# Kernel tuning notes

Measured on AMD Instinct MI355X. Metric: run time of the kernel, lower is better.

Reference implementation:

```python
import jax, jax.numpy as jnp
import numpy as np

B, D, K = 8192, 512, 4096
MAX_WORD_LENGTH = 16
RESIDUAL_THRESHOLD = 0.01
DECAY_FACTOR = 0.95
EPS_TARGET = 1e-8


def setup_inputs() -> dict:
    key = jax.random.key(0)
    k1, k2 = jax.random.split(key)
    targets = jax.random.normal(k1, (B, D), dtype=jnp.float32)
    codebook = jax.random.normal(k2, (K, D), dtype=jnp.float32)
    return {"targets": targets, "codebook": codebook}


def reference(targets, codebook):
    """Batched greedy residual pursuit (allow_negative_signs=True).

    Returns:
      seq      [B, L] int32 signed indices (>=0: add idx; <0: subtract (-idx-1)); 0 where inactive
      mask     [B, L] bool, True where a step actually emitted a symbol
      residual [B, D] final residual after pursuit
    """
    target_norm = jnp.linalg.norm(targets, axis=-1)  # [B]

    def step(residual, step_idx):
        rnorm = jnp.linalg.norm(residual, axis=-1)  # [B]
        active = (rnorm >= RESIDUAL_THRESHOLD) & (target_norm >= EPS_TARGET)
        # cosine similarity of each codebook vector with residual direction
        res_dir = residual / jnp.maximum(rnorm, 1e-12)[:, None]
        cos = jnp.einsum('bd,kd->bk', res_dir, codebook)  # [B, K]
        best = jnp.argmax(jnp.abs(cos), axis=-1)  # [B]
        best_cos = jnp.take_along_axis(cos, best[:, None], axis=-1)[:, 0]
        signed = jnp.where(best_cos >= 0, best, -(best + 1)).astype(jnp.int32)
        sign = jnp.where(best_cos >= 0, 1.0, -1.0).astype(residual.dtype)
        decay = jnp.power(jnp.asarray(DECAY_FACTOR, residual.dtype),
                          (step_idx + 1).astype(residual.dtype))
        contrib = sign[:, None] * decay * codebook[best]  # [B, D]
        new_res = jnp.where(active[:, None], residual - contrib, residual)
        out_idx = jnp.where(active, signed, 0)
        return new_res, (out_idx, active)

    residual, (seq, mask) = jax.lax.scan(step, targets, jnp.arange(MAX_WORD_LENGTH))
    return seq.T, mask.T, residual
```

## Files before the change

### kernel.cpp

```cpp
#include <hip/hip_runtime.h>
#include <hip/hip_bf16.h>

#define B_SZ 8192
#define D_SZ 512
#define K_SZ 4096
#define L_SZ 16
#define M_ALL (B_SZ + K_SZ)

typedef __attribute__((ext_vector_type(8))) short short8v;
typedef __attribute__((ext_vector_type(4))) float f32x4;
typedef _Float16 half8v __attribute__((ext_vector_type(8)));
typedef _Float16 h2 __attribute__((ext_vector_type(2)));
struct H2x4 { h2 a, b, c, d; };

typedef const __attribute__((address_space(1))) void gvoid;
typedef __attribute__((address_space(3))) void lvoid;

static __device__ __forceinline__ h2 habs2(h2 a) {
    unsigned u = __builtin_bit_cast(unsigned, a) & 0x7FFF7FFFu;
    return __builtin_bit_cast(h2, u);
}
static __device__ __forceinline__ h2 hmax2(h2 a, h2 b) {
#if __has_builtin(__builtin_elementwise_max)
    return __builtin_elementwise_max(a, b);
#else
    h2 r; r[0] = a[0] > b[0] ? a[0] : b[0]; r[1] = a[1] > b[1] ? a[1] : b[1]; return r;
#endif
}

__global__ void cast_bf16_kernel(const float* __restrict__ targets,
                                 const float* __restrict__ codebook,
                                 __hip_bfloat16* __restrict__ abf) {
    int idx = blockIdx.x * blockDim.x + threadIdx.x;
    const int total4 = (M_ALL * D_SZ) / 4;
    if (idx >= total4) return;
    int base = idx * 4;
    const float* src = (base < B_SZ * D_SZ) ? (targets + base)
                                            : (codebook + (base - B_SZ * D_SZ));
    float4 v = *(const float4*)src;
    abf[base + 0] = __float2bfloat16(v.x);
    abf[base + 1] = __float2bfloat16(v.y);
    abf[base + 2] = __float2bfloat16(v.z);
    abf[base + 3] = __float2bfloat16(v.w);
}

__global__ void cn2_kernel(const float* __restrict__ codebook,
                           double* __restrict__ cn2) {
    int row  = blockIdx.x * 4 + (threadIdx.x >> 6);
    int lane = threadIdx.x & 63;
    const float* r = codebook + (size_t)row * D_SZ;
    double s = 0.0;
#pragma unroll
    for (int j = 0; j < 8; j++) { double v = (double)r[lane + 64 * j]; s += v * v; }
#pragma unroll
    for (int o = 32; o > 0; o >>= 1) s += __shfl_down(s, o, 64);
    if (lane == 0) cn2[row] = s;
}

#define BM 128
#define BN 128
#define BK 32

__global__ __launch_bounds__(256)
void gemm_bt_kernel(const __hip_bfloat16* __restrict__ A,
                    const __hip_bfloat16* __restrict__ Bm,
                    _Float16* __restrict__ C) {
    __shared__ short As[BM * BK];
    __shared__ short Bs[BN * BK];
    const int tid  = threadIdx.x;
    const int bm   = blockIdx.y * BM;
    const int bn   = blockIdx.x * BN;
    const int wave = tid >> 6, lane = tid & 63;
    const int wm = (wave & 1) * 64, wn = (wave >> 1) * 64;
    const int row16 = lane & 15, quad = lane >> 4;
    const int koff = quad * 8;

    f32x4 acc[4][4] = {};

    const short* Ag = (const short*)A;
    const short* Bg = (const short*)Bm;
    const int srow = lane >> 2;
    const int scol = (lane & 3) * 8;

    for (int k0 = 0; k0 < D_SZ; k0 += BK) {
        __syncthreads();
#pragma unroll
        for (int c = 0; c < 2; c++) {
            int row = (wave * 2 + c) * 16 + srow;
            __builtin_amdgcn_global_load_lds(
                (gvoid*)(Ag + (size_t)(bm + row) * D_SZ + k0 + scol),
                (lvoid*)(As + row * BK + scol), 16, 0, 0);
            __builtin_amdgcn_global_load_lds(
                (gvoid*)(Bg + (size_t)(bn + row) * D_SZ + k0 + scol),
                (lvoid*)(Bs + row * BK + scol), 16, 0, 0);
        }
        __syncthreads();

        short8v af[4], bf[4];
#pragma unroll
        for (int i = 0; i < 4; i++)
            af[i] = *(const short8v*)(As + (wm + i * 16 + row16) * BK + koff);
#pragma unroll
        for (int j = 0; j < 4; j++)
            bf[j] = *(const short8v*)(Bs + (wn + j * 16 + row16) * BK + koff);
#pragma unroll
        for (int i = 0; i < 4; i++)
#pragma unroll
            for (int j = 0; j < 4; j++)
                acc[i][j] = __builtin_amdgcn_mfma_f32_16x16x32_bf16(af[i], bf[j], acc[i][j], 0, 0, 0);
    }

    if (bm < B_SZ) {
#pragma unroll
        for (int i = 0; i < 4; i++) {
            int grow = bm + wm + i * 16 + quad * 4;
#pragma unroll
            for (int j = 0; j < 4; j++) {
                int gcol = bn + wn + j * 16 + row16;
#pragma unroll
                for (int r = 0; r < 4; r++)
                    __builtin_nontemporal_store((_Float16)acc[i][j][r],
                                                &C[(size_t)(grow + r) * K_SZ + gcol]);
            }
        }
    } else {
#pragma unroll
        for (int i = 0; i < 4; i++) {
            int grow = bm + wm + i * 16 + quad * 4;
#pragma unroll
            for (int j = 0; j < 4; j++) {
                int gcol = bn + wn + j * 16 + row16;
#pragma unroll
                for (int r = 0; r < 4; r++)
                    C[(size_t)(grow + r) * K_SZ + gcol] = (_Float16)acc[i][j][r];
            }
        }
    }
}

#define MAXC 16
#define MARGIN 1.5f

__global__ __launch_bounds__(256, 4)
void pursuit_kernel(const float* __restrict__ targets,
                    const float* __restrict__ codebook,
                    const _Float16* __restrict__ S,
                    const double* __restrict__ cn2,
                    float* __restrict__ out) {
    const int wave = threadIdx.x >> 6;
    const int lane = threadIdx.x & 63;
    const int b = blockIdx.x * 4 + wave;
    const int lane8 = lane * 8;

    __shared__ alignas(16) _Float16 g_s[4][K_SZ];
    __shared__ int s_cnt[4];
    __shared__ int s_cand[4][MAXC];
    _Float16* g = g_s[wave];
    int* cnt  = &s_cnt[wave];
    int* cand = s_cand[wave];

    h2 tmax; tmax[0] = (_Float16)0; tmax[1] = (_Float16)0;
    {
        const _Float16* g0 = S + (size_t)b * K_SZ + lane8;
#pragma unroll
        for (int c = 0; c < 8; c++) {
            half8v h = __builtin_nontemporal_load((const half8v*)(g0 + c * 512));
            *(half8v*)&g[c * 512 + lane8] = h;
            H2x4 u = __builtin_bit_cast(H2x4, h);
            tmax = hmax2(tmax, hmax2(hmax2(habs2(u.a), habs2(u.b)),
                                     hmax2(habs2(u.c), habs2(u.d))));
        }
    }
    float m = fmaxf((float)tmax[0], (float)tmax[1]);

    double rres[8];
    double loc = 0.0;
    {
        const float* tg = targets + (size_t)b * D_SZ + lane8;
        f32x4 t0 = __builtin_nontemporal_load((const f32x4*)tg);
        f32x4 t1 = __builtin_nontemporal_load((const f32x4*)(tg + 4));
        rres[0] = t0[0]; rres[1] = t0[1]; rres[2] = t0[2]; rres[3] = t0[3];
        rres[4] = t1[0]; rres[5] = t1[1]; rres[6] = t1[2]; rres[7] = t1[3];
#pragma unroll
        for (int e = 0; e < 8; e++) loc += rres[e] * rres[e];
    }
#pragma unroll
    for (int o = 32; o > 0; o >>= 1) loc += __shfl_xor(loc, o, 64);
    double rn2 = loc;
    const bool tgt_ok = (sqrt(loc) >= 1e-8);

    float* out_seq  = out + (size_t)b * L_SZ;
    float* out_mask = out + (size_t)B_SZ * L_SZ + (size_t)b * L_SZ;
    float* out_res  = out + (size_t)2 * B_SZ * L_SZ + (size_t)b * D_SZ;

    double decay = 1.0;

    for (int t = 0; t < L_SZ; t++) {
        decay *= 0.95;
        bool active = (sqrt(rn2) >= 0.01) && tgt_ok;
        if (!active) {
            if (lane == 0)
                for (int tt = t; tt < L_SZ; tt++) {
                    __builtin_nontemporal_store(0.0f, &out_seq[tt]);
                    __builtin_nontemporal_store(0.0f, &out_mask[tt]);
                }
            break;
        }

        float M = m;
#pragma unroll
        for (int o = 32; o > 0; o >>= 1) M = fmaxf(M, __shfl_xor(M, o, 64));
        float thr = M - MARGIN;

        if (lane == 0) *cnt = 0;
        if (m >= thr) {
#pragma unroll
            for (int c = 0; c < 8; c++) {
                half8v h = *(const half8v*)&g[c * 512 + lane8];
#pragma unroll
                for (int e = 0; e < 8; e++) {
                    float f = fabsf((float)h[e]);
                    if (f >= thr) {
                        int q = atomicAdd(cnt, 1);
                        if (q < MAXC) cand[q] = c * 512 + lane8 + e;
                    }
                }
            }
        }
        __threadfence_block();
        int nc = min(*cnt, MAXC);

        int bk; double bv;
        float4 c0, c1;
        half8v Gh[8];
        if (nc == 1) {
            bk = __builtin_amdgcn_readfirstlane(cand[0]);
            const float* cr = codebook + (size_t)bk * D_SZ + lane8;
            const _Float16* Gp = S + (size_t)(B_SZ + bk) * K_SZ + lane8;
            c0 = *(const float4*)cr;
            c1 = *(const float4*)(cr + 4);
#pragma unroll
            for (int c = 0; c < 8; c++) Gh[c] = *(const half8v*)(Gp + c * 512);
            double s = rres[0] * (double)c0.x + rres[1] * (double)c0.y
                     + rres[2] * (double)c0.z + rres[3] * (double)c0.w
                     + rres[4] * (double)c1.x + rres[5] * (double)c1.y
                     + rres[6] * (double)c1.z + rres[7] * (double)c1.w;
#pragma unroll
            for (int o = 32; o > 0; o >>= 1) s += __shfl_xor(s, o, 64);
            bv = s;
        } else {
            bk = -1; bv = 0.0;
            for (int ci = 0; ci < nc; ci++) {
                int k = __builtin_amdgcn_readfirstlane(cand[ci]);
                const float* cr = codebook + (size_t)k * D_SZ + lane8;
                float4 d0 = *(const float4*)cr;
                float4 d1 = *(const float4*)(cr + 4);
                double s = rres[0] * (double)d0.x + rres[1] * (double)d0.y
                         + rres[2] * (double)d0.z + rres[3] * (double)d0.w
                         + rres[4] * (double)d1.x + rres[5] * (double)d1.y
                         + rres[6] * (double)d1.z + rres[7] * (double)d1.w;
#pragma unroll
                for (int o = 32; o > 0; o >>= 1) s += __shfl_xor(s, o, 64);
                if (bk < 0 || fabs(s) > fabs(bv) ||
                    (fabs(s) == fabs(bv) && k < bk)) { bk = k; bv = s; }
            }
            const float* cr = codebook + (size_t)bk * D_SZ + lane8;
            const _Float16* Gp = S + (size_t)(B_SZ + bk) * K_SZ + lane8;
            c0 = *(const float4*)cr;
            c1 = *(const float4*)(cr + 4);
#pragma unroll
            for (int c = 0; c < 8; c++) Gh[c] = *(const half8v*)(Gp + c * 512);
        }

        const double cn2bk = cn2[bk];
        double sd = ((bv >= 0.0) ? 1.0 : -1.0) * decay;
        rn2 = rn2 - 2.0 * sd * bv + sd * sd * cn2bk;
        if (lane == 0) {
            __builtin_nontemporal_store((float)((bv >= 0.0) ? bk : (-bk - 1)), &out_seq[t]);
            __builtin_nontemporal_store(1.0f, &out_mask[t]);
        }
        const float sdf = (float)sd;
        h2 sdh2; sdh2[0] = (_Float16)sdf; sdh2[1] = (_Float16)sdf;

        tmax[0] = (_Float16)0; tmax[1] = (_Float16)0;
#pragma unroll
        for (int c = 0; c < 8; c++) {
            half8v gv = *(const half8v*)&g[c * 512 + lane8];
            H2x4 ug = __builtin_bit_cast(H2x4, gv);
            H2x4 uG = __builtin_bit_cast(H2x4, Gh[c]);
            ug.a -= sdh2 * uG.a; ug.b -= sdh2 * uG.b;
            ug.c -= sdh2 * uG.c; ug.d -= sdh2 * uG.d;
            *(half8v*)&g[c * 512 + lane8] = __builtin_bit_cast(half8v, ug);
            tmax = hmax2(tmax, hmax2(hmax2(habs2(ug.a), habs2(ug.b)),
                                     hmax2(habs2(ug.c), habs2(ug.d))));
        }
        m = fmaxf((float)tmax[0], (float)tmax[1]);

        if (lane == 0) g[bk] = (_Float16)(float)(bv - sd * cn2bk);

        rres[0] -= sd * (double)c0.x; rres[1] -= sd * (double)c0.y;
        rres[2] -= sd * (double)c0.z; rres[3] -= sd * (double)c0.w;
        rres[4] -= sd * (double)c1.x; rres[5] -= sd * (double)c1.y;
        rres[6] -= sd * (double)c1.z; rres[7] -= sd * (double)c1.w;
    }

    {
        f32x4 r0, r1;
        r0[0] = (float)rres[0]; r0[1] = (float)rres[1]; r0[2] = (float)rres[2]; r0[3] = (float)rres[3];
        r1[0] = (float)rres[4]; r1[1] = (float)rres[5]; r1[2] = (float)rres[6]; r1[3] = (float)rres[7];
        __builtin_nontemporal_store(r0, (f32x4*)(out_res + lane8));
        __builtin_nontemporal_store(r1, (f32x4*)(out_res + lane8 + 4));
    }
}

extern "C" void kernel_launch(void* const* d_in, const int* in_sizes, int n_in,
                              void* d_out, int out_size, void* d_ws, size_t ws_size,
                              hipStream_t stream) {
    const float* targets  = (const float*)d_in[0];
    const float* codebook = (const float*)d_in[1];
    float* out = (float*)d_out;

    __hip_bfloat16* abf = (__hip_bfloat16*)d_ws;
    _Float16* S = (_Float16*)((char*)d_ws + (size_t)M_ALL * D_SZ * 2);
    double* cn2 = (double*)((char*)d_ws + (size_t)M_ALL * D_SZ * 2
                                        + (size_t)M_ALL * K_SZ * 2);

    int total4 = (M_ALL * D_SZ) / 4;
    cast_bf16_kernel<<<(total4 + 255) / 256, 256, 0, stream>>>(targets, codebook, abf);
    cn2_kernel<<<K_SZ / 4, 256, 0, stream>>>(codebook, cn2);

    dim3 ggrid(K_SZ / BN, M_ALL / BM);
    gemm_bt_kernel<<<ggrid, 256, 0, stream>>>(abf, abf + (size_t)B_SZ * D_SZ, S);

    pursuit_kernel<<<B_SZ / 4, 256, 0, stream>>>(targets, codebook, S, cn2, out);
}
```

Before: 335.5 us.

## Use ballot-based single-candidate fast path and per-chunk maxima in pursuit step

Keeps per-chunk max magnitudes so candidate scanning only rereads LDS chunks that can exceed the threshold. When exactly one lane holds exactly one candidate, it is taken through wave ballot and shuffles instead of LDS atomics and fences. When the Gram max is large, the sign is taken from the fp16 Gram value, so the Gram update can start before the fp64 dot product completes. The general path now prefetches the row of the largest-Gram candidate and refetches only if the exact check picks a different one. This adds register pressure, and trusting the fp16 sign is a small accuracy risk.

```diff
diff --git a/kernel.cpp b/kernel.cpp
--- a/kernel.cpp
+++ b/kernel.cpp
@@ -153,25 +153,31 @@
     const int lane8 = lane * 8;
 
     __shared__ alignas(16) _Float16 g_s[4][K_SZ];
-    __shared__ int s_cnt[4];
-    __shared__ int s_cand[4][MAXC];
+    __shared__ int   s_cnt[4];
+    __shared__ int   s_ci[4][MAXC];
+    __shared__ float s_cv[4][MAXC];
     _Float16* g = g_s[wave];
-    int* cnt  = &s_cnt[wave];
-    int* cand = s_cand[wave];
-
-    h2 tmax; tmax[0] = (_Float16)0; tmax[1] = (_Float16)0;
+    int* cnt = &s_cnt[wave];
+    int* ci  = s_ci[wave];
+    float* cv = s_cv[wave];
+
+    float gmf[8];
+    float m;
+
     {
         const _Float16* g0 = S + (size_t)b * K_SZ + lane8;
+        m = 0.0f;
 #pragma unroll
         for (int c = 0; c < 8; c++) {
             half8v h = __builtin_nontemporal_load((const half8v*)(g0 + c * 512));
             *(half8v*)&g[c * 512 + lane8] = h;
             H2x4 u = __builtin_bit_cast(H2x4, h);
-            tmax = hmax2(tmax, hmax2(hmax2(habs2(u.a), habs2(u.b)),
-                                     hmax2(habs2(u.c), habs2(u.d))));
-        }
-    }
-    float m = fmaxf((float)tmax[0], (float)tmax[1]);
+            h2 gm2 = hmax2(hmax2(habs2(u.a), habs2(u.b)),
+                           hmax2(habs2(u.c), habs2(u.d)));
+            gmf[c] = fmaxf((float)gm2[0], (float)gm2[1]);
+            m = fmaxf(m, gmf[c]);
+        }
+    }
 
     double rres[8];
     double loc = 0.0;
@@ -192,6 +198,33 @@
     float* out_seq  = out + (size_t)b * L_SZ;
     float* out_mask = out + (size_t)B_SZ * L_SZ + (size_t)b * L_SZ;
     float* out_res  = out + (size_t)2 * B_SZ * L_SZ + (size_t)b * D_SZ;
+
+    auto edot = [&](const float4& a0, const float4& a1) -> double {
+        double s = rres[0] * (double)a0.x + rres[1] * (double)a0.y
+                 + rres[2] * (double)a0.z + rres[3] * (double)a0.w
+                 + rres[4] * (double)a1.x + rres[5] * (double)a1.y
+                 + rres[6] * (double)a1.z + rres[7] * (double)a1.w;
+#pragma unroll
+        for (int o = 32; o > 0; o >>= 1) s += __shfl_xor(s, o, 64);
+        return s;
+    };
+
+    auto upd = [&](const half8v* Gh, h2 sdh2) {
+        m = 0.0f;
+#pragma unroll
+        for (int c = 0; c < 8; c++) {
+            half8v gv = *(const half8v*)&g[c * 512 + lane8];
+            H2x4 ug = __builtin_bit_cast(H2x4, gv);
+            H2x4 uG = __builtin_bit_cast(H2x4, Gh[c]);
+            ug.a -= sdh2 * uG.a; ug.b -= sdh2 * uG.b;
+            ug.c -= sdh2 * uG.c; ug.d -= sdh2 * uG.d;
+            *(half8v*)&g[c * 512 + lane8] = __builtin_bit_cast(half8v, ug);
+            h2 gm2 = hmax2(hmax2(habs2(ug.a), habs2(ug.b)),
+                           hmax2(habs2(ug.c), habs2(ug.d)));
+            gmf[c] = fmaxf((float)gm2[0], (float)gm2[1]);
+            m = fmaxf(m, gmf[c]);
+        }
+    };
 
     double decay = 1.0;
 
@@ -212,89 +245,117 @@
         for (int o = 32; o > 0; o >>= 1) M = fmaxf(M, __shfl_xor(M, o, 64));
         float thr = M - MARGIN;
 
-        if (lane == 0) *cnt = 0;
+        unsigned long long mask = __ballot(m >= thr);
+        int npl = __popcll(mask);
+        int src = __ffsll((long long)mask) - 1;
+
+        int lcnt = 0, lidx = 0; float lval = 0.0f;
         if (m >= thr) {
 #pragma unroll
-            for (int c = 0; c < 8; c++) {
-                half8v h = *(const half8v*)&g[c * 512 + lane8];
-#pragma unroll
-                for (int e = 0; e < 8; e++) {
-                    float f = fabsf((float)h[e]);
-                    if (f >= thr) {
-                        int q = atomicAdd(cnt, 1);
-                        if (q < MAXC) cand[q] = c * 512 + lane8 + e;
+            for (int c = 0; c < 8; c++)
+                if (gmf[c] >= thr) {
+                    half8v h = *(const half8v*)&g[c * 512 + lane8];
+#pragma unroll
+                    for (int e = 0; e < 8; e++) {
+                        float f = (float)h[e];
+                        if (fabsf(f) >= thr) { lcnt++; lidx = c * 512 + lane8 + e; lval = f; }
                     }
                 }
-            }
-        }
-        __threadfence_block();
-        int nc = min(*cnt, MAXC);
-
-        int bk; double bv;
-        float4 c0, c1;
+        }
+
+        bool fast = false;
+        int bk = 0; float gval = 0.0f; int nc = 1;
+        if (npl == 1) {
+            int cw = __shfl(lcnt, src, 64);
+            if (cw == 1) {
+                fast = true;
+                bk   = __builtin_amdgcn_readfirstlane(__shfl(lidx, src, 64));
+                gval = __shfl(lval, src, 64);
+            }
+        }
+        if (!fast) {
+            if (lane == 0) *cnt = 0;
+            __threadfence_block();
+            if (lcnt > 0) {
+#pragma unroll
+                for (int c = 0; c < 8; c++)
+                    if (gmf[c] >= thr) {
+                        half8v h = *(const half8v*)&g[c * 512 + lane8];
+#pragma unroll
+                        for (int e = 0; e < 8; e++) {
+                            float f = (float)h[e];
+                            if (fabsf(f) >= thr) {
+                                int q = atomicAdd(cnt, 1);
+                                if (q < MAXC) { ci[q] = c * 512 + lane8 + e; cv[q] = f; }
+                            }
+                        }
+                    }
+            }
+            __threadfence_block();
+            nc = min(*cnt, MAXC);
+            bk = __builtin_amdgcn_readfirstlane(ci[0]); gval = cv[0];
+            for (int q = 1; q < nc; q++) {
+                float v = cv[q];
+                if (fabsf(v) > fabsf(gval)) { gval = v; bk = __builtin_amdgcn_readfirstlane(ci[q]); }
+            }
+        }
+
+        const float* cr = codebook + (size_t)bk * D_SZ + lane8;
+        const _Float16* Gp = S + (size_t)(B_SZ + bk) * K_SZ + lane8;
+        float4 c0 = *(const float4*)cr;
+        float4 c1 = *(const float4*)(cr + 4);
         half8v Gh[8];
-        if (nc == 1) {
-            bk = __builtin_amdgcn_readfirstlane(cand[0]);
-            const float* cr = codebook + (size_t)bk * D_SZ + lane8;
-            const _Float16* Gp = S + (size_t)(B_SZ + bk) * K_SZ + lane8;
-            c0 = *(const float4*)cr;
-            c1 = *(const float4*)(cr + 4);
-#pragma unroll
-            for (int c = 0; c < 8; c++) Gh[c] = *(const half8v*)(Gp + c * 512);
-            double s = rres[0] * (double)c0.x + rres[1] * (double)c0.y
-                     + rres[2] * (double)c0.z + rres[3] * (double)c0.w
-                     + rres[4] * (double)c1.x + rres[5] * (double)c1.y
-                     + rres[6] * (double)c1.z + rres[7] * (double)c1.w;
-#pragma unroll
-            for (int o = 32; o > 0; o >>= 1) s += __shfl_xor(s, o, 64);
-            bv = s;
+#pragma unroll
+        for (int c = 0; c < 8; c++) Gh[c] = *(const half8v*)(Gp + c * 512);
+
+        double bv, sd;
+        if (fast) {
+            if (M >= 4.0f) {
+                sd = ((gval >= 0.0f) ? 1.0 : -1.0) * decay;
+                float sdf = (float)sd;
+                h2 sdh2; sdh2[0] = (_Float16)sdf; sdh2[1] = (_Float16)sdf;
+                upd(Gh, sdh2);
+                bv = edot(c0, c1);
+            } else {
+                bv = edot(c0, c1);
+                sd = ((bv >= 0.0) ? 1.0 : -1.0) * decay;
+                float sdf = (float)sd;
+                h2 sdh2; sdh2[0] = (_Float16)sdf; sdh2[1] = (_Float16)sdf;
+                upd(Gh, sdh2);
+            }
         } else {
-            bk = -1; bv = 0.0;
-            for (int ci = 0; ci < nc; ci++) {
-                int k = __builtin_amdgcn_readfirstlane(cand[ci]);
-                const float* cr = codebook + (size_t)k * D_SZ + lane8;
-                float4 d0 = *(const float4*)cr;
-                float4 d1 = *(const float4*)(cr + 4);
-                double s = rres[0] * (double)d0.x + rres[1] * (double)d0.y
-                         + rres[2] * (double)d0.z + rres[3] * (double)d0.w
-                         + rres[4] * (double)d1.x + rres[5] * (double)d1.y
-                         + rres[6] * (double)d1.z + rres[7] * (double)d1.w;
-#pragma unroll
-                for (int o = 32; o > 0; o >>= 1) s += __shfl_xor(s, o, 64);
-                if (bk < 0 || fabs(s) > fabs(bv) ||
-                    (fabs(s) == fabs(bv) && k < bk)) { bk = k; bv = s; }
-            }
-            const float* cr = codebook + (size_t)bk * D_SZ + lane8;
-            const _Float16* Gp = S + (size_t)(B_SZ + bk) * K_SZ + lane8;
-            c0 = *(const float4*)cr;
-            c1 = *(const float4*)(cr + 4);
-#pragma unroll
-            for (int c = 0; c < 8; c++) Gh[c] = *(const half8v*)(Gp + c * 512);
+            int wk = -1; double wv = 0.0;
+            for (int q = 0; q < nc; q++) {
+                int k = __builtin_amdgcn_readfirstlane(ci[q]);
+                const float* kr = codebook + (size_t)k * D_SZ + lane8;
+                float4 d0 = *(const float4*)kr;
+                float4 d1 = *(const float4*)(kr + 4);
+                double s = edot(d0, d1);
+                if (wk < 0 || fabs(s) > fabs(wv) ||
+                    (fabs(s) == fabs(wv) && k < wk)) { wk = k; wv = s; }
+            }
+            if (wk != bk) {
+                bk = wk;
+                const float* wr = codebook + (size_t)bk * D_SZ + lane8;
+                const _Float16* Wp = S + (size_t)(B_SZ + bk) * K_SZ + lane8;
+                c0 = *(const float4*)wr;
+                c1 = *(const float4*)(wr + 4);
+#pragma unroll
+                for (int c = 0; c < 8; c++) Gh[c] = *(const half8v*)(Wp + c * 512);
+            }
+            bv = wv;
+            sd = ((bv >= 0.0) ? 1.0 : -1.0) * decay;
+            float sdf = (float)sd;
+            h2 sdh2; sdh2[0] = (_Float16)sdf; sdh2[1] = (_Float16)sdf;
+            upd(Gh, sdh2);
         }
 
         const double cn2bk = cn2[bk];
-        double sd = ((bv >= 0.0) ? 1.0 : -1.0) * decay;
         rn2 = rn2 - 2.0 * sd * bv + sd * sd * cn2bk;
         if (lane == 0) {
             __builtin_nontemporal_store((float)((bv >= 0.0) ? bk : (-bk - 1)), &out_seq[t]);
             __builtin_nontemporal_store(1.0f, &out_mask[t]);
         }
-        const float sdf = (float)sd;
-        h2 sdh2; sdh2[0] = (_Float16)sdf; sdh2[1] = (_Float16)sdf;
-
-        tmax[0] = (_Float16)0; tmax[1] = (_Float16)0;
-#pragma unroll
-        for (int c = 0; c < 8; c++) {
-            half8v gv = *(const half8v*)&g[c * 512 + lane8];
-            H2x4 ug = __builtin_bit_cast(H2x4, gv);
-            H2x4 uG = __builtin_bit_cast(H2x4, Gh[c]);
-            ug.a -= sdh2 * uG.a; ug.b -= sdh2 * uG.b;
-            ug.c -= sdh2 * uG.c; ug.d -= sdh2 * uG.d;
-            *(half8v*)&g[c * 512 + lane8] = __builtin_bit_cast(half8v, ug);
-            tmax = hmax2(tmax, hmax2(hmax2(habs2(ug.a), habs2(ug.b)),
-                                     hmax2(habs2(ug.c), habs2(ug.d))));
-        }
-        m = fmaxf((float)tmax[0], (float)tmax[1]);
 
         if (lane == 0) g[bk] = (_Float16)(float)(bv - sd * cn2bk);
 
```

Measured after the change: 336.4 us. Within noise of the previous version (+0.3%).
